# Performance work log

Measured on AMD Instinct MI355X. Metric: run time of the kernel, lower is better.

## Reference

```python
import jax, jax.numpy as jnp
import numpy as np

SELECTED_NUM = 4096
BN_EPS = 1e-5


def _conv1d(x, w, pad):
    # x: [B, C_in, L], w: [C_out, C_in, K]
    return jax.lax.conv_general_dilated(
        x, w, window_strides=(1,), padding=[(pad, pad)],
        dimension_numbers=('NCH', 'OIH', 'NCH'))


def _bn(x, g, b, m, v):
    # eval-mode BatchNorm1d over channel dim of [B, C, L]
    inv = g / jnp.sqrt(v + BN_EPS)
    return x * inv[None, :, None] + (b - m * inv)[None, :, None]


def setup_inputs() -> dict:
    key = jax.random.key(0)
    ks = jax.random.split(key, 16)
    B, N, CODE, NCLS = 4, 262144, 7, 3
    inp = {
        'box_preds': jax.random.normal(ks[0], (B, N, CODE), jnp.float32),
        'cls_preds': jax.random.normal(ks[1], (B, N, NCLS), jnp.float32),
        # conv_share: Conv1d(10,32,3) + BN(32) + ReLU + Conv1d(32,64,3) + BN(64) + ReLU
        'conv1_w': jax.random.normal(ks[2], (32, 10, 3), jnp.float32) * 0.1,
        'bn1_g': jax.random.uniform(ks[3], (32,), jnp.float32, 0.5, 1.5),
        'bn1_b': jax.random.normal(ks[4], (32,), jnp.float32) * 0.1,
        'bn1_m': jax.random.normal(ks[5], (32,), jnp.float32) * 0.1,
        'bn1_v': jax.random.uniform(ks[6], (32,), jnp.float32, 0.5, 1.5),
        'conv2_w': jax.random.normal(ks[7], (64, 32, 3), jnp.float32) * 0.1,
        'bn2_g': jax.random.uniform(ks[8], (64,), jnp.float32, 0.5, 1.5),
        'bn2_b': jax.random.normal(ks[9], (64,), jnp.float32) * 0.1,
        'bn2_m': jax.random.normal(ks[10], (64,), jnp.float32) * 0.1,
        'bn2_v': jax.random.uniform(ks[11], (64,), jnp.float32, 0.5, 1.5),
        # heads: Conv1d(64,5,1,bias=True), Conv1d(64,1,1,bias=True)
        'bin_w': jax.random.normal(ks[12], (5, 64, 1), jnp.float32) * 0.1,
        'bin_b': jnp.full((5,), -float(np.log((1 - 0.01) / 0.01)), jnp.float32),
        'res_w': jax.random.normal(ks[13], (1, 64, 1), jnp.float32) * 0.001,
        'res_b': jnp.zeros((1,), jnp.float32),
    }
    return inp


def reference(box_preds, cls_preds, conv1_w, bn1_g, bn1_b, bn1_m, bn1_v,
              conv2_w, bn2_g, bn2_b, bn2_m, bn2_v, bin_w, bin_b, res_w, res_b):
    # ---- proposal_layer: per-batch sigmoid(max-cls-score) topk + gather ----
    score = jax.nn.sigmoid(jnp.max(cls_preds, axis=-1))          # [B, N]
    _, sel = jax.lax.top_k(score, SELECTED_NUM)                  # [B, K]
    box_sel = jnp.take_along_axis(box_preds, sel[:, :, None], axis=1)  # [B, K, 7]
    cls_sel = jnp.take_along_axis(cls_preds, sel[:, :, None], axis=1)  # [B, K, 3]

    # ---- conv_share + heads over channel-first layout [B, 10, K] ----
    x = jnp.concatenate([box_sel, cls_sel], axis=-1).transpose(0, 2, 1)  # [B, 10, K]
    x = jax.nn.relu(_bn(_conv1d(x, conv1_w, 1), bn1_g, bn1_b, bn1_m, bn1_v))
    x = jax.nn.relu(_bn(_conv1d(x, conv2_w, 1), bn2_g, bn2_b, bn2_m, bn2_v))  # [B, 64, K]

    iou_bin = _conv1d(x, bin_w, 0) + bin_b[None, :, None]        # [B, 5, K]
    iou_res = _conv1d(x, res_w, 0) + res_b[None, :, None]        # [B, 1, K]

    iou_preds_bin = iou_bin.transpose(0, 2, 1)                   # [B, K, 5]
    iou_preds_residual = iou_res.transpose(0, 2, 1)              # [B, K, 1]
    return iou_preds_bin, iou_preds_residual, box_sel, cls_sel
```

## Files before the change

kernel.cpp:

```cpp
#include <hip/hip_runtime.h>
#include <stdint.h>

#define NPTS 262144
#define NB 4
#define KSEL 4096
#define CAP 8192
#define SLICE_LEN 1024
#define CBLK 128
#define HBLK 64
#define NBIN 8192

#define OFF_BITS  0ULL
#define OFF_H13   (4ULL*NPTS*NB)
#define OFF_CTRL  (OFF_H13 + 4ULL*NBIN*NB)
#define OFF_GRANK (OFF_CTRL + 1024ULL)
#define OFF_CAND  (OFF_GRANK + 4ULL*CAP*NB)
#define WS_NEEDED (OFF_CAND + 8ULL*CAP*NB)

#define OBIN 0
#define ORES (NB*KSEL*5)
#define OBOX (ORES + NB*KSEL)
#define OCLS (OBOX + NB*KSEL*7)


__device__ __forceinline__ uint32_t key_of(float mx) {
    uint32_t b = __float_as_uint(mx);
    uint32_t mask = ((int32_t)b >> 31) | 0x80000000u;
    return b ^ mask;
}

__device__ __forceinline__ void suffix_scan_256(volatile uint32_t* part, int tid) {
    #pragma unroll
    for (int off = 1; off < 256; off <<= 1) {
        uint32_t v = part[tid] + ((tid + off < 256) ? part[tid + off] : 0u);
        __syncthreads();
        part[tid] = v;
        __syncthreads();
    }
}

__global__ __launch_bounds__(256) void k_init(uint4* __restrict__ h13v)
{
    h13v[blockIdx.x * 256 + threadIdx.x] = make_uint4(0u, 0u, 0u, 0u);
}

__global__ __launch_bounds__(256) void k_score(
    const float* __restrict__ cls, uint32_t* __restrict__ bits, uint32_t* __restrict__ h13,
    uint32_t* __restrict__ grank, uint32_t* __restrict__ ctrl)
{
    __shared__ uint32_t lh[NBIN];
    for (int i = threadIdx.x; i < NBIN; i += 256) lh[i] = 0;
    __syncthreads();
    int b = blockIdx.y, bx = blockIdx.x;
    for (int it = 0; it < 4; ++it) {
        int chunk = bx * 1024 + it * 256 + threadIdx.x;
        const float4* p = (const float4*)(cls + ((size_t)b * NPTS + (size_t)chunk * 4) * 3);
        float4 v0 = p[0], v1 = p[1], v2 = p[2];
        uint4 o;
        o.x = key_of(fmaxf(fmaxf(v0.x, v0.y), v0.z));
        o.y = key_of(fmaxf(fmaxf(v0.w, v1.x), v1.y));
        o.z = key_of(fmaxf(fmaxf(v1.z, v1.w), v2.x));
        o.w = key_of(fmaxf(fmaxf(v2.y, v2.z), v2.w));
        ((uint4*)(bits + (size_t)b * NPTS))[chunk] = o;
        atomicAdd(&lh[o.x >> 19], 1u);
        atomicAdd(&lh[o.y >> 19], 1u);
        atomicAdd(&lh[o.z >> 19], 1u);
        atomicAdd(&lh[o.w >> 19], 1u);
    }
    if (bx == 1) {
        uint4* zg = (uint4*)(grank + (size_t)b * CAP);
        #pragma unroll
        for (int i = 0; i < 8; ++i) zg[threadIdx.x + i * 256] = make_uint4(0u, 0u, 0u, 0u);
    } else if (bx == 2 && threadIdx.x == 0) {
        ctrl[b * 16 + 3] = 0u;
    }
    __syncthreads();
    uint32_t* h13b = h13 + (size_t)b * NBIN;
    for (int i = threadIdx.x; i < NBIN; i += 256) {
        uint32_t c = lh[i];
        if (c) atomicAdd(&h13b[i], c);
    }
}

__global__ __launch_bounds__(256) void k_compact(
    const uint32_t* __restrict__ bits, const uint32_t* __restrict__ h13,
    uint32_t* __restrict__ ctrl, uint64_t* __restrict__ cand)
{
    __shared__ uint32_t bins[NBIN];
    __shared__ uint32_t part[257];
    __shared__ uint32_t segS, Ts;
    __shared__ uint32_t wbase[4];
    int b = blockIdx.y, bx = blockIdx.x;
    int tid = threadIdx.x;
    const uint4* src = (const uint4*)(h13 + (size_t)b * NBIN);
    for (int i = tid; i < NBIN / 4; i += 256) ((uint4*)bins)[i] = src[i];
    __syncthreads();
    {
        uint32_t s = 0;
        int base2 = tid * 32;
        #pragma unroll
        for (int j = 0; j < 32; ++j) s += bins[base2 + j];
        part[tid] = s;
        if (tid == 0) part[256] = 0u;
    }
    __syncthreads();
    suffix_scan_256(part, tid);
    {
        uint32_t si = part[tid], sn = part[tid + 1];
        if (si >= (uint32_t)KSEL && sn < (uint32_t)KSEL) segS = (uint32_t)tid;
    }
    __syncthreads();
    if (tid < 32) {
        uint32_t seg = segS;
        uint32_t above = part[seg + 1];
        uint32_t cnt = above;
        for (int j = 31; j >= tid; --j) cnt += bins[seg * 32 + j];
        uint32_t cntn = cnt - bins[seg * 32 + tid];
        if (cnt >= (uint32_t)KSEL && cntn < (uint32_t)KSEL)
            Ts = seg * 32 + (uint32_t)tid;
    }
    __syncthreads();
    const uint32_t T = Ts;
    const int lane = tid & 63, wave = tid >> 6;
    const uint64_t lmask = (1ull << lane) - 1ull;

    int chunk0 = bx * 512 + tid;
    const uint4* sb = (const uint4*)(bits + (size_t)b * NPTS);
    uint4 v0 = sb[chunk0];
    uint4 v1 = sb[chunk0 + 256];
    uint32_t ks[8] = {v0.x, v0.y, v0.z, v0.w, v1.x, v1.y, v1.z, v1.w};
    bool sel[8];
    #pragma unroll
    for (int i = 0; i < 8; ++i) sel[i] = (ks[i] >> 19) >= T;

    uint32_t wsum = 0;
    #pragma unroll
    for (int i = 0; i < 8; ++i) wsum += (uint32_t)__popcll(__ballot(sel[i]));
    if (lane == 0) wbase[wave] = wsum;
    __syncthreads();
    if (tid == 0) {
        uint32_t c0 = wbase[0], c1 = wbase[1], c2 = wbase[2], c3 = wbase[3];
        uint32_t tot = c0 + c1 + c2 + c3;
        uint32_t base = tot ? atomicAdd(&ctrl[b * 16 + 3], tot) : 0u;
        wbase[0] = base;
        wbase[1] = base + c0;
        wbase[2] = base + c0 + c1;
        wbase[3] = base + c0 + c1 + c2;
    }
    __syncthreads();
    uint32_t off = wbase[wave];
    #pragma unroll
    for (int i = 0; i < 8; ++i) {
        uint64_t m = __ballot(sel[i]);
        if (sel[i]) {
            uint32_t pos = off + (uint32_t)__popcll(m & lmask);
            uint32_t n = (uint32_t)(chunk0 + (i < 4 ? 0 : 256)) * 4 + (uint32_t)(i & 3);
            if (pos < CAP)
                cand[(size_t)b * CAP + pos] = ((uint64_t)(~ks[i]) << 32) | (uint64_t)n;
        }
        off += (uint32_t)__popcll(m);
    }
}

__global__ __launch_bounds__(256) void k_rank1(
    const uint64_t* __restrict__ cand, const uint32_t* __restrict__ ctrl,
    uint32_t* __restrict__ grank)
{
    __shared__ uint64_t keys[SLICE_LEN];
    int b = blockIdx.z;
    uint32_t C = ctrl[b * 16 + 3];
    if (C > CAP) C = CAP;
    uint32_t ig0 = blockIdx.x * 256;
    uint32_t sk0 = blockIdx.y * SLICE_LEN;
    if (ig0 >= C || sk0 >= C) return;
    uint32_t nk = C - sk0; if (nk > SLICE_LEN) nk = SLICE_LEN;
    const uint64_t* cb = cand + (size_t)b * CAP;
    for (uint32_t i = threadIdx.x; i < nk; i += 256) keys[i] = cb[sk0 + i];
    __syncthreads();
    uint32_t item = ig0 + threadIdx.x;
    if (item >= C) return;
    uint64_t me = cb[item];
    uint32_t r = 0;
    #pragma unroll 16
    for (uint32_t i = 0; i < nk; ++i) r += (keys[i] < me) ? 1u : 0u;
    atomicAdd(&grank[b * CAP + item], r);
}

__global__ __launch_bounds__(256) void k_rank2(
    const uint64_t* __restrict__ cand, const uint32_t* __restrict__ ctrl,
    const uint32_t* __restrict__ grank,
    const float* __restrict__ box, const float* __restrict__ cls, float* __restrict__ out)
{
    int b = blockIdx.y;
    uint32_t C = ctrl[b * 16 + 3];
    if (C > CAP) C = CAP;
    uint32_t item = blockIdx.x * 256 + threadIdx.x;
    if (blockIdx.x * 256 >= C) return;
    if (item >= C) return;
    uint64_t me = cand[(size_t)b * CAP + item];
    uint32_t rank = grank[b * CAP + item];
    if (rank < KSEL) {
        uint32_t n = (uint32_t)me;
        const float* bp = box + ((size_t)b * NPTS + n) * 7;
        float* ob = out + OBOX + ((size_t)b * KSEL + rank) * 7;
        #pragma unroll
        for (int c = 0; c < 7; ++c) ob[c] = bp[c];
        const float* cp = cls + ((size_t)b * NPTS + n) * 3;
        float* oc = out + OCLS + ((size_t)b * KSEL + rank) * 3;
        #pragma unroll
        for (int c = 0; c < 3; ++c) oc[c] = cp[c];
    }
}

__global__ __launch_bounds__(256) void k_conv(
    const float* __restrict__ c1w, const float* __restrict__ g1v, const float* __restrict__ b1v,
    const float* __restrict__ m1v, const float* __restrict__ v1v,
    const float* __restrict__ c2w, const float* __restrict__ g2v, const float* __restrict__ b2v,
    const float* __restrict__ m2v, const float* __restrict__ v2v,
    const float* __restrict__ binw, const float* __restrict__ binb,
    const float* __restrict__ resw, const float* __restrict__ resb,
    float* __restrict__ out)
{
    __shared__ __align__(16) float w1s[960];
    __shared__ __align__(16) float b1s[32];
    __shared__ __align__(16) float w2s[6144];
    __shared__ __align__(16) float b2s[64];
    __shared__ __align__(16) float hws[6][64];
    __shared__ __align__(16) float xin[10][80];
    __shared__ __align__(16) float x1s[32][68];
    __shared__ __align__(16) float x2t[64][68];

    int tid = threadIdx.x;
    int b = blockIdx.y;
    int tile0 = blockIdx.x * 64;
    const float* boxsel = out + OBOX + (size_t)b * KSEL * 7;
    const float* clssel = out + OCLS + (size_t)b * KSEL * 3;

    for (int t = tid; t < 960; t += 256) {
        int c = t / 30, r = t - c * 30, i = r / 3, tap = r - i * 3;
        float inv = g1v[c] * rsqrtf(v1v[c] + 1e-5f);
        w1s[(i * 3 + tap) * 32 + c] = c1w[t] * inv;
    }
    if (tid < 32) {
        float inv = g1v[tid] * rsqrtf(v1v[tid] + 1e-5f);
        b1s[tid] = b1v[tid] - m1v[tid] * inv;
    }
    for (int t = tid; t < 6144; t += 256) {
        int o = t / 96, r = t - o * 96, i = r / 3, tap = r - i * 3;
        float inv = g2v[o] * rsqrtf(v2v[o] + 1e-5f);
        w2s[(i * 3 + tap) * 64 + o] = c2w[t] * inv;
    }
    if (tid >= 64 && tid < 128) {
        int o = tid - 64;
        float inv = g2v[o] * rsqrtf(v2v[o] + 1e-5f);
        b2s[o] = b2v[o] - m2v[o] * inv;
    }
    for (int t = tid; t < 384; t += 256)
        ((float*)hws)[t] = (t < 320) ? binw[t] : resw[t - 320];

    for (int u = tid; u < 680; u += 256) {
        int c = u / 68, k2 = u - c * 68;
        int g = tile0 + k2 - 2;
        float val = 0.f;
        if (g >= 0 && g < KSEL) val = (c < 7) ? boxsel[g * 7 + c] : clssel[g * 3 + (c - 7)];
        xin[c][k2] = val;
    }
    __syncthreads();

    {
        int c = tid & 31, kg = tid >> 5;
        int k0 = kg * 9;
        int nk = 66 - k0; if (nk > 9) nk = 9;
        float a[9];
        #pragma unroll
        for (int kk = 0; kk < 9; ++kk) a[kk] = b1s[c];
        #pragma unroll 2
        for (int i = 0; i < 10; ++i) {
            float xv[11];
            #pragma unroll
            for (int j = 0; j < 11; ++j) xv[j] = xin[i][k0 + j];
            #pragma unroll
            for (int tap = 0; tap < 3; ++tap) {
                float w = w1s[(i * 3 + tap) * 32 + c];
                #pragma unroll
                for (int kk = 0; kk < 9; ++kk) a[kk] = fmaf(w, xv[kk + tap], a[kk]);
            }
        }
        for (int kk = 0; kk < nk; ++kk) {
            int k = k0 + kk, gp = tile0 + k - 1;
            x1s[c][k] = (gp >= 0 && gp < KSEL) ? fmaxf(a[kk], 0.f) : 0.f;
        }
    }
    __syncthreads();

    {
        int o = tid & 63, pg = tid >> 6;
        int p0 = pg * 16;
        float acc[16];
        float bz = b2s[o];
        #pragma unroll
        for (int kk = 0; kk < 16; ++kk) acc[kk] = bz;
        #pragma unroll 4
        for (int i = 0; i < 32; ++i) {
            float4 xq[5];
            const float4* xr = (const float4*)&x1s[i][p0];
            #pragma unroll
            for (int q = 0; q < 5; ++q) xq[q] = xr[q];
            const float* xf = (const float*)xq;
            float w0 = w2s[(i * 3 + 0) * 64 + o];
            float w1 = w2s[(i * 3 + 1) * 64 + o];
            float w2 = w2s[(i * 3 + 2) * 64 + o];
            #pragma unroll
            for (int kk = 0; kk < 16; ++kk) {
                float t0 = fmaf(w0, xf[kk], acc[kk]);
                t0 = fmaf(w1, xf[kk + 1], t0);
                acc[kk] = fmaf(w2, xf[kk + 2], t0);
            }
        }
        #pragma unroll
        for (int kk = 0; kk < 16; ++kk)
            x2t[p0 + kk][o] = fmaxf(acc[kk], 0.f);
    }
    __syncthreads();

    {
        int p = tid & 63, g = tid >> 6;
        const float4* xr = (const float4*)&x2t[p][0];
        const float4* hw4 = (const float4*)hws;
        size_t gpos = (size_t)b * KSEL + (size_t)(tile0 + p);
        if (g < 2) {
            int j0 = g * 2, j1 = j0 + 1;
            float s0 = 0.f, s1 = 0.f;
            #pragma unroll
            for (int q = 0; q < 16; ++q) {
                float4 xv = xr[q];
                float4 wa = hw4[j0 * 16 + q];
                float4 wb = hw4[j1 * 16 + q];
                s0 = fmaf(xv.x, wa.x, s0); s0 = fmaf(xv.y, wa.y, s0);
                s0 = fmaf(xv.z, wa.z, s0); s0 = fmaf(xv.w, wa.w, s0);
                s1 = fmaf(xv.x, wb.x, s1); s1 = fmaf(xv.y, wb.y, s1);
                s1 = fmaf(xv.z, wb.z, s1); s1 = fmaf(xv.w, wb.w, s1);
            }
            out[OBIN + gpos * 5 + j0] = s0 + binb[j0];
            out[OBIN + gpos * 5 + j1] = s1 + binb[j1];
        } else {
            int j = (g == 2) ? 4 : 5;
            float s = 0.f;
            #pragma unroll
            for (int q = 0; q < 16; ++q) {
                float4 xv = xr[q];
                float4 wa = hw4[j * 16 + q];
                s = fmaf(xv.x, wa.x, s); s = fmaf(xv.y, wa.y, s);
                s = fmaf(xv.z, wa.z, s); s = fmaf(xv.w, wa.w, s);
            }
            if (g == 2) out[OBIN + gpos * 5 + 4] = s + binb[4];
            else        out[ORES + gpos]         = s + resb[0];
        }
    }
}

extern "C" void kernel_launch(void* const* d_in, const int* in_sizes, int n_in,
                              void* d_out, int out_size, void* d_ws, size_t ws_size,
                              hipStream_t stream)
{
    const float* box  = (const float*)d_in[0];
    const float* cls  = (const float*)d_in[1];
    const float* c1w  = (const float*)d_in[2];
    const float* g1   = (const float*)d_in[3];
    const float* b1   = (const float*)d_in[4];
    const float* m1   = (const float*)d_in[5];
    const float* v1   = (const float*)d_in[6];
    const float* c2w  = (const float*)d_in[7];
    const float* g2   = (const float*)d_in[8];
    const float* b2   = (const float*)d_in[9];
    const float* m2   = (const float*)d_in[10];
    const float* v2   = (const float*)d_in[11];
    const float* binw = (const float*)d_in[12];
    const float* binb = (const float*)d_in[13];
    const float* resw = (const float*)d_in[14];
    const float* resb = (const float*)d_in[15];
    float* out = (float*)d_out;
    char* ws = (char*)d_ws;
    if (ws_size < WS_NEEDED) return;

    uint32_t* bits  = (uint32_t*)(ws + OFF_BITS);
    uint32_t* h13   = (uint32_t*)(ws + OFF_H13);
    uint32_t* ctrl  = (uint32_t*)(ws + OFF_CTRL);
    uint32_t* grank = (uint32_t*)(ws + OFF_GRANK);
    uint64_t* cand  = (uint64_t*)(ws + OFF_CAND);

    k_init<<<(NBIN * NB) / 1024, 256, 0, stream>>>((uint4*)h13);
    k_score<<<dim3(HBLK, NB), 256, 0, stream>>>(cls, bits, h13, grank, ctrl);
    k_compact<<<dim3(CBLK, NB), 256, 0, stream>>>(bits, h13, ctrl, cand);
    k_rank1<<<dim3(CAP / 256, 8, NB), 256, 0, stream>>>(cand, ctrl, grank);
    k_rank2<<<dim3(CAP / 256, NB), 256, 0, stream>>>(cand, ctrl, grank, box, cls, out);
    k_conv<<<dim3(64, NB), 256, 0, stream>>>(c1w, g1, b1, m1, v1, c2w, g2, b2, m2, v2,
                                             binw, binb, resw, resb, out);
}
```

Measured before the change: 68.48 us.

## Fuse threshold search and gather via last-block-done atomic counters

Moves the histogram threshold search into the score kernel: the last block per batch, found with an atomic counter, scans the global histogram and writes the threshold to ctrl. This stops every compact block from reloading and rescanning the full histogram. The rank and gather kernels are merged the same way: the last slice block per item group does the gather. One kernel launch is removed, in exchange for extra fences, atomics and a serial tail on the last block.

```diff
diff --git a/kernel.cpp b/kernel.cpp
--- a/kernel.cpp
+++ b/kernel.cpp
@@ -39,9 +39,11 @@
     }
 }
 
-__global__ __launch_bounds__(256) void k_init(uint4* __restrict__ h13v)
-{
-    h13v[blockIdx.x * 256 + threadIdx.x] = make_uint4(0u, 0u, 0u, 0u);
+__global__ __launch_bounds__(256) void k_init(uint4* __restrict__ h13v, uint32_t* __restrict__ ctrl)
+{
+    int bx = blockIdx.x, tid = threadIdx.x;
+    h13v[bx * 256 + tid] = make_uint4(0u, 0u, 0u, 0u);
+    if (bx == 0) ctrl[tid] = 0u;
 }
 
 __global__ __launch_bounds__(256) void k_score(
@@ -49,11 +51,14 @@
     uint32_t* __restrict__ grank, uint32_t* __restrict__ ctrl)
 {
     __shared__ uint32_t lh[NBIN];
-    for (int i = threadIdx.x; i < NBIN; i += 256) lh[i] = 0;
-    __syncthreads();
-    int b = blockIdx.y, bx = blockIdx.x;
+    __shared__ uint32_t part[257];
+    __shared__ uint32_t segS;
+    __shared__ int amLastS;
+    int b = blockIdx.y, bx = blockIdx.x, tid = threadIdx.x;
+    for (int i = tid; i < NBIN; i += 256) lh[i] = 0;
+    __syncthreads();
     for (int it = 0; it < 4; ++it) {
-        int chunk = bx * 1024 + it * 256 + threadIdx.x;
+        int chunk = bx * 1024 + it * 256 + tid;
         const float4* p = (const float4*)(cls + ((size_t)b * NPTS + (size_t)chunk * 4) * 3);
         float4 v0 = p[0], v1 = p[1], v2 = p[2];
         uint4 o;
@@ -70,36 +75,30 @@
     if (bx == 1) {
         uint4* zg = (uint4*)(grank + (size_t)b * CAP);
         #pragma unroll
-        for (int i = 0; i < 8; ++i) zg[threadIdx.x + i * 256] = make_uint4(0u, 0u, 0u, 0u);
-    } else if (bx == 2 && threadIdx.x == 0) {
-        ctrl[b * 16 + 3] = 0u;
+        for (int i = 0; i < 8; ++i) zg[tid + i * 256] = make_uint4(0u, 0u, 0u, 0u);
     }
     __syncthreads();
     uint32_t* h13b = h13 + (size_t)b * NBIN;
-    for (int i = threadIdx.x; i < NBIN; i += 256) {
+    for (int i = tid; i < NBIN; i += 256) {
         uint32_t c = lh[i];
         if (c) atomicAdd(&h13b[i], c);
     }
-}
-
-__global__ __launch_bounds__(256) void k_compact(
-    const uint32_t* __restrict__ bits, const uint32_t* __restrict__ h13,
-    uint32_t* __restrict__ ctrl, uint64_t* __restrict__ cand)
-{
-    __shared__ uint32_t bins[NBIN];
-    __shared__ uint32_t part[257];
-    __shared__ uint32_t segS, Ts;
-    __shared__ uint32_t wbase[4];
-    int b = blockIdx.y, bx = blockIdx.x;
-    int tid = threadIdx.x;
-    const uint4* src = (const uint4*)(h13 + (size_t)b * NBIN);
-    for (int i = tid; i < NBIN / 4; i += 256) ((uint4*)bins)[i] = src[i];
+    __threadfence();
+    if (tid == 0) {
+        uint32_t r = atomicAdd(&ctrl[b * 64 + 15], 1u);
+        amLastS = (r == (uint32_t)(HBLK - 1));
+    }
+    __syncthreads();
+    if (!amLastS) return;
+
+    for (int i = tid; i < NBIN / 4; i += 256)
+        ((uint4*)lh)[i] = ((const uint4*)h13b)[i];
     __syncthreads();
     {
         uint32_t s = 0;
         int base2 = tid * 32;
         #pragma unroll
-        for (int j = 0; j < 32; ++j) s += bins[base2 + j];
+        for (int j = 0; j < 32; ++j) s += lh[base2 + j];
         part[tid] = s;
         if (tid == 0) part[256] = 0u;
     }
@@ -114,13 +113,19 @@
         uint32_t seg = segS;
         uint32_t above = part[seg + 1];
         uint32_t cnt = above;
-        for (int j = 31; j >= tid; --j) cnt += bins[seg * 32 + j];
-        uint32_t cntn = cnt - bins[seg * 32 + tid];
+        for (int j = 31; j >= tid; --j) cnt += lh[seg * 32 + j];
+        uint32_t cntn = cnt - lh[seg * 32 + tid];
         if (cnt >= (uint32_t)KSEL && cntn < (uint32_t)KSEL)
-            Ts = seg * 32 + (uint32_t)tid;
-    }
-    __syncthreads();
-    const uint32_t T = Ts;
+            ctrl[b * 64 + 2] = seg * 32 + (uint32_t)tid;
+    }
+}
+
+__global__ __launch_bounds__(256) void k_compact(
+    const uint32_t* __restrict__ bits, uint32_t* __restrict__ ctrl, uint64_t* __restrict__ cand)
+{
+    __shared__ uint32_t wbase[4];
+    int b = blockIdx.y, bx = blockIdx.x, tid = threadIdx.x;
+    const uint32_t T = ctrl[b * 64 + 2];
     const int lane = tid & 63, wave = tid >> 6;
     const uint64_t lmask = (1ull << lane) - 1ull;
 
@@ -141,7 +146,7 @@
     if (tid == 0) {
         uint32_t c0 = wbase[0], c1 = wbase[1], c2 = wbase[2], c3 = wbase[3];
         uint32_t tot = c0 + c1 + c2 + c3;
-        uint32_t base = tot ? atomicAdd(&ctrl[b * 16 + 3], tot) : 0u;
+        uint32_t base = tot ? atomicAdd(&ctrl[b * 64 + 3], tot) : 0u;
         wbase[0] = base;
         wbase[1] = base + c0;
         wbase[2] = base + c0 + c1;
@@ -162,53 +167,52 @@
     }
 }
 
-__global__ __launch_bounds__(256) void k_rank1(
-    const uint64_t* __restrict__ cand, const uint32_t* __restrict__ ctrl,
-    uint32_t* __restrict__ grank)
+__global__ __launch_bounds__(256) void k_rank(
+    const uint64_t* __restrict__ cand, uint32_t* __restrict__ ctrl,
+    uint32_t* __restrict__ grank,
+    const float* __restrict__ box, const float* __restrict__ cls, float* __restrict__ out)
 {
     __shared__ uint64_t keys[SLICE_LEN];
-    int b = blockIdx.z;
-    uint32_t C = ctrl[b * 16 + 3];
+    __shared__ int lastS;
+    int b = blockIdx.z, tid = threadIdx.x;
+    uint32_t C = ctrl[b * 64 + 3];
     if (C > CAP) C = CAP;
-    uint32_t ig0 = blockIdx.x * 256;
+    uint32_t ig = blockIdx.x;
+    uint32_t ig0 = ig * 256;
     uint32_t sk0 = blockIdx.y * SLICE_LEN;
     if (ig0 >= C || sk0 >= C) return;
+    uint32_t Sact = (C + SLICE_LEN - 1) / SLICE_LEN;
     uint32_t nk = C - sk0; if (nk > SLICE_LEN) nk = SLICE_LEN;
     const uint64_t* cb = cand + (size_t)b * CAP;
-    for (uint32_t i = threadIdx.x; i < nk; i += 256) keys[i] = cb[sk0 + i];
-    __syncthreads();
-    uint32_t item = ig0 + threadIdx.x;
-    if (item >= C) return;
-    uint64_t me = cb[item];
+    for (uint32_t i = tid; i < nk; i += 256) keys[i] = cb[sk0 + i];
+    __syncthreads();
+    uint32_t item = ig0 + tid;
+    uint64_t me = (item < C) ? cb[item] : ~0ull;
     uint32_t r = 0;
     #pragma unroll 16
     for (uint32_t i = 0; i < nk; ++i) r += (keys[i] < me) ? 1u : 0u;
-    atomicAdd(&grank[b * CAP + item], r);
-}
-
-__global__ __launch_bounds__(256) void k_rank2(
-    const uint64_t* __restrict__ cand, const uint32_t* __restrict__ ctrl,
-    const uint32_t* __restrict__ grank,
-    const float* __restrict__ box, const float* __restrict__ cls, float* __restrict__ out)
-{
-    int b = blockIdx.y;
-    uint32_t C = ctrl[b * 16 + 3];
-    if (C > CAP) C = CAP;
-    uint32_t item = blockIdx.x * 256 + threadIdx.x;
-    if (blockIdx.x * 256 >= C) return;
-    if (item >= C) return;
-    uint64_t me = cand[(size_t)b * CAP + item];
-    uint32_t rank = grank[b * CAP + item];
-    if (rank < KSEL) {
-        uint32_t n = (uint32_t)me;
-        const float* bp = box + ((size_t)b * NPTS + n) * 7;
-        float* ob = out + OBOX + ((size_t)b * KSEL + rank) * 7;
-        #pragma unroll
-        for (int c = 0; c < 7; ++c) ob[c] = bp[c];
-        const float* cp = cls + ((size_t)b * NPTS + n) * 3;
-        float* oc = out + OCLS + ((size_t)b * KSEL + rank) * 3;
-        #pragma unroll
-        for (int c = 0; c < 3; ++c) oc[c] = cp[c];
+    if (item < C) atomicAdd(&grank[b * CAP + item], r);
+    __syncthreads();
+    __threadfence();
+    if (tid == 0) {
+        uint32_t old = atomicAdd(&ctrl[b * 64 + 16 + ig], 1u);
+        lastS = (old == Sact - 1);
+    }
+    __syncthreads();
+    if (!lastS) return;
+    if (item < C) {
+        uint32_t rank = grank[b * CAP + item];
+        if (rank < KSEL) {
+            uint32_t n = (uint32_t)cb[item];
+            const float* bp = box + ((size_t)b * NPTS + n) * 7;
+            float* ob = out + OBOX + ((size_t)b * KSEL + rank) * 7;
+            #pragma unroll
+            for (int c = 0; c < 7; ++c) ob[c] = bp[c];
+            const float* cp = cls + ((size_t)b * NPTS + n) * 3;
+            float* oc = out + OCLS + ((size_t)b * KSEL + rank) * 3;
+            #pragma unroll
+            for (int c = 0; c < 3; ++c) oc[c] = cp[c];
+        }
     }
 }
 
@@ -389,11 +393,10 @@
     uint32_t* grank = (uint32_t*)(ws + OFF_GRANK);
     uint64_t* cand  = (uint64_t*)(ws + OFF_CAND);
 
-    k_init<<<(NBIN * NB) / 1024, 256, 0, stream>>>((uint4*)h13);
+    k_init<<<(NBIN * NB) / 1024, 256, 0, stream>>>((uint4*)h13, ctrl);
     k_score<<<dim3(HBLK, NB), 256, 0, stream>>>(cls, bits, h13, grank, ctrl);
-    k_compact<<<dim3(CBLK, NB), 256, 0, stream>>>(bits, h13, ctrl, cand);
-    k_rank1<<<dim3(CAP / 256, 8, NB), 256, 0, stream>>>(cand, ctrl, grank);
-    k_rank2<<<dim3(CAP / 256, NB), 256, 0, stream>>>(cand, ctrl, grank, box, cls, out);
+    k_compact<<<dim3(CBLK, NB), 256, 0, stream>>>(bits, ctrl, cand);
+    k_rank<<<dim3(CAP / 256, 8, NB), 256, 0, stream>>>(cand, ctrl, grank, box, cls, out);
     k_conv<<<dim3(64, NB), 256, 0, stream>>>(c1w, g1, b1, m1, v1, c2w, g2, b2, m2, v2,
                                              binw, binb, resw, resb, out);
 }
```

After: 99.30 us. 1.45x slower.

## Bucket candidates by histogram bin to restrict rank counting to same-bin keys

Applied to the files above, without the earlier changes.

Candidates are now written into bin-sorted positions in compaction. Each slot comes from a per-bin global counter plus a suffix sum of the histogram, replacing the single atomic cursor. The rank kernel then only compares each candidate against keys in its own bin range, not all candidates, and writes ranks directly without atomics. This drops the quadratic all-pairs comparison and the grank zeroing. The cost is extra shared memory, per-bin global atomics, and a serial suffix loop per selected element in compaction.

```diff
diff --git a/kernel.cpp b/kernel.cpp
--- a/kernel.cpp
+++ b/kernel.cpp
@@ -12,10 +12,12 @@
 
 #define OFF_BITS  0ULL
 #define OFF_H13   (4ULL*NPTS*NB)
-#define OFF_CTRL  (OFF_H13 + 4ULL*NBIN*NB)
-#define OFF_GRANK (OFF_CTRL + 1024ULL)
-#define OFF_CAND  (OFF_GRANK + 4ULL*CAP*NB)
-#define WS_NEEDED (OFF_CAND + 8ULL*CAP*NB)
+#define OFF_SFX   (OFF_H13 + 4ULL*NBIN*NB)
+#define OFF_BCNT  (OFF_SFX + 4ULL*NBIN*NB)
+#define OFF_CTRL  (OFF_BCNT + 4ULL*NBIN*NB)
+#define OFF_CAND  (OFF_CTRL + 1024ULL)
+#define OFF_GRANK (OFF_CAND + 8ULL*CAP*NB)
+#define WS_NEEDED (OFF_GRANK + 4ULL*CAP*NB)
 
 #define OBIN 0
 #define ORES (NB*KSEL*5)
@@ -39,21 +41,23 @@
     }
 }
 
-__global__ __launch_bounds__(256) void k_init(uint4* __restrict__ h13v)
-{
-    h13v[blockIdx.x * 256 + threadIdx.x] = make_uint4(0u, 0u, 0u, 0u);
+__global__ __launch_bounds__(256) void k_init(uint4* __restrict__ h13v, uint4* __restrict__ bcntv)
+{
+    int bx = blockIdx.x, tid = threadIdx.x;
+    uint4 z = make_uint4(0u, 0u, 0u, 0u);
+    if (bx < 32) h13v[bx * 256 + tid] = z;
+    else         bcntv[(bx - 32) * 256 + tid] = z;
 }
 
 __global__ __launch_bounds__(256) void k_score(
-    const float* __restrict__ cls, uint32_t* __restrict__ bits, uint32_t* __restrict__ h13,
-    uint32_t* __restrict__ grank, uint32_t* __restrict__ ctrl)
+    const float* __restrict__ cls, uint32_t* __restrict__ bits, uint32_t* __restrict__ h13)
 {
     __shared__ uint32_t lh[NBIN];
-    for (int i = threadIdx.x; i < NBIN; i += 256) lh[i] = 0;
-    __syncthreads();
-    int b = blockIdx.y, bx = blockIdx.x;
+    int b = blockIdx.y, bx = blockIdx.x, tid = threadIdx.x;
+    for (int i = tid; i < NBIN; i += 256) lh[i] = 0;
+    __syncthreads();
     for (int it = 0; it < 4; ++it) {
-        int chunk = bx * 1024 + it * 256 + threadIdx.x;
+        int chunk = bx * 1024 + it * 256 + tid;
         const float4* p = (const float4*)(cls + ((size_t)b * NPTS + (size_t)chunk * 4) * 3);
         float4 v0 = p[0], v1 = p[1], v2 = p[2];
         uint4 o;
@@ -67,16 +71,9 @@
         atomicAdd(&lh[o.z >> 19], 1u);
         atomicAdd(&lh[o.w >> 19], 1u);
     }
-    if (bx == 1) {
-        uint4* zg = (uint4*)(grank + (size_t)b * CAP);
-        #pragma unroll
-        for (int i = 0; i < 8; ++i) zg[threadIdx.x + i * 256] = make_uint4(0u, 0u, 0u, 0u);
-    } else if (bx == 2 && threadIdx.x == 0) {
-        ctrl[b * 16 + 3] = 0u;
-    }
     __syncthreads();
     uint32_t* h13b = h13 + (size_t)b * NBIN;
-    for (int i = threadIdx.x; i < NBIN; i += 256) {
+    for (int i = tid; i < NBIN; i += 256) {
         uint32_t c = lh[i];
         if (c) atomicAdd(&h13b[i], c);
     }
@@ -84,16 +81,17 @@
 
 __global__ __launch_bounds__(256) void k_compact(
     const uint32_t* __restrict__ bits, const uint32_t* __restrict__ h13,
+    uint32_t* __restrict__ sfx, uint32_t* __restrict__ bcnt,
     uint32_t* __restrict__ ctrl, uint64_t* __restrict__ cand)
 {
     __shared__ uint32_t bins[NBIN];
+    __shared__ uint32_t lha[NBIN];
     __shared__ uint32_t part[257];
     __shared__ uint32_t segS, Ts;
-    __shared__ uint32_t wbase[4];
-    int b = blockIdx.y, bx = blockIdx.x;
-    int tid = threadIdx.x;
+    int b = blockIdx.y, bx = blockIdx.x, tid = threadIdx.x;
     const uint4* src = (const uint4*)(h13 + (size_t)b * NBIN);
     for (int i = tid; i < NBIN / 4; i += 256) ((uint4*)bins)[i] = src[i];
+    for (int i = tid; i < NBIN; i += 256) lha[i] = 0;
     __syncthreads();
     {
         uint32_t s = 0;
@@ -121,8 +119,19 @@
     }
     __syncthreads();
     const uint32_t T = Ts;
-    const int lane = tid & 63, wave = tid >> 6;
-    const uint64_t lmask = (1ull << lane) - 1ull;
+    if (bx == 0) {
+        uint32_t run = part[tid + 1];
+        uint32_t* sb2 = sfx + (size_t)b * NBIN + tid * 32;
+        for (int j = 31; j >= 0; --j) {
+            run += bins[tid * 32 + j];
+            sb2[j] = run;
+        }
+        if (tid == 0) {
+            uint32_t seg = T >> 5, run2 = part[seg + 1];
+            for (int j = 31; j >= (int)(T & 31u); --j) run2 += bins[seg * 32 + j];
+            ctrl[b * 64 + 3] = (run2 > (uint32_t)CAP) ? (uint32_t)CAP : run2;
+        }
+    }
 
     int chunk0 = bx * 512 + tid;
     const uint4* sb = (const uint4*)(bits + (size_t)b * NPTS);
@@ -133,57 +142,78 @@
     #pragma unroll
     for (int i = 0; i < 8; ++i) sel[i] = (ks[i] >> 19) >= T;
 
-    uint32_t wsum = 0;
     #pragma unroll
-    for (int i = 0; i < 8; ++i) wsum += (uint32_t)__popcll(__ballot(sel[i]));
-    if (lane == 0) wbase[wave] = wsum;
-    __syncthreads();
-    if (tid == 0) {
-        uint32_t c0 = wbase[0], c1 = wbase[1], c2 = wbase[2], c3 = wbase[3];
-        uint32_t tot = c0 + c1 + c2 + c3;
-        uint32_t base = tot ? atomicAdd(&ctrl[b * 16 + 3], tot) : 0u;
-        wbase[0] = base;
-        wbase[1] = base + c0;
-        wbase[2] = base + c0 + c1;
-        wbase[3] = base + c0 + c1 + c2;
-    }
-    __syncthreads();
-    uint32_t off = wbase[wave];
+    for (int i = 0; i < 8; ++i)
+        if (sel[i]) atomicAdd(&lha[ks[i] >> 19], 1u);
+    __syncthreads();
+    {
+        uint32_t* bc = bcnt + (size_t)b * NBIN;
+        for (int i = tid; i < NBIN; i += 256) {
+            uint32_t c = lha[i];
+            if (c) lha[i] = atomicAdd(&bc[i], c);
+        }
+    }
+    __syncthreads();
     #pragma unroll
     for (int i = 0; i < 8; ++i) {
-        uint64_t m = __ballot(sel[i]);
         if (sel[i]) {
-            uint32_t pos = off + (uint32_t)__popcll(m & lmask);
+            uint32_t bin = ks[i] >> 19;
+            uint32_t lo = 0;
+            if (bin < NBIN - 1) {
+                uint32_t x = bin + 1, seg = x >> 5;
+                lo = part[seg + 1];
+                for (int j = 31; j >= (int)(x & 31u); --j) lo += bins[seg * 32 + j];
+            }
+            uint32_t pos = lo + atomicAdd(&lha[bin], 1u);
             uint32_t n = (uint32_t)(chunk0 + (i < 4 ? 0 : 256)) * 4 + (uint32_t)(i & 3);
             if (pos < CAP)
                 cand[(size_t)b * CAP + pos] = ((uint64_t)(~ks[i]) << 32) | (uint64_t)n;
         }
-        off += (uint32_t)__popcll(m);
     }
 }
 
 __global__ __launch_bounds__(256) void k_rank1(
     const uint64_t* __restrict__ cand, const uint32_t* __restrict__ ctrl,
-    uint32_t* __restrict__ grank)
+    const uint32_t* __restrict__ sfx, uint32_t* __restrict__ grank)
 {
     __shared__ uint64_t keys[SLICE_LEN];
-    int b = blockIdx.z;
-    uint32_t C = ctrl[b * 16 + 3];
+    __shared__ uint32_t loMinS, hiMaxS;
+    int b = blockIdx.y, tid = threadIdx.x;
+    uint32_t C = ctrl[b * 64 + 3];
     if (C > CAP) C = CAP;
     uint32_t ig0 = blockIdx.x * 256;
-    uint32_t sk0 = blockIdx.y * SLICE_LEN;
-    if (ig0 >= C || sk0 >= C) return;
-    uint32_t nk = C - sk0; if (nk > SLICE_LEN) nk = SLICE_LEN;
+    if (ig0 >= C) return;
     const uint64_t* cb = cand + (size_t)b * CAP;
-    for (uint32_t i = threadIdx.x; i < nk; i += 256) keys[i] = cb[sk0 + i];
-    __syncthreads();
-    uint32_t item = ig0 + threadIdx.x;
-    if (item >= C) return;
-    uint64_t me = cb[item];
-    uint32_t r = 0;
-    #pragma unroll 16
-    for (uint32_t i = 0; i < nk; ++i) r += (keys[i] < me) ? 1u : 0u;
-    atomicAdd(&grank[b * CAP + item], r);
+    uint32_t item = ig0 + tid;
+    bool valid = (item < C);
+    uint64_t me = valid ? cb[item] : ~0ull;
+    uint32_t ksv = ~(uint32_t)(me >> 32);
+    uint32_t bin = ksv >> 19;
+    const uint32_t* sfb = sfx + (size_t)b * NBIN;
+    uint32_t lo = 0, hi = 0;
+    if (valid) {
+        lo = (bin >= NBIN - 1) ? 0u : sfb[bin + 1];
+        hi = sfb[bin];
+        if (lo > C) lo = C;
+        if (hi > C) hi = C;
+    }
+    if (tid == 0) { loMinS = 0xFFFFFFFFu; hiMaxS = 0u; }
+    __syncthreads();
+    if (valid) { atomicMin(&loMinS, lo); atomicMax(&hiMaxS, hi); }
+    __syncthreads();
+    uint32_t r = lo;
+    for (uint32_t s0 = loMinS; s0 < hiMaxS; s0 += SLICE_LEN) {
+        uint32_t nk = hiMaxS - s0; if (nk > SLICE_LEN) nk = SLICE_LEN;
+        for (uint32_t i = tid; i < nk; i += 256) keys[i] = cb[s0 + i];
+        __syncthreads();
+        if (valid && hi > s0 && lo < s0 + nk) {
+            uint32_t a = (lo > s0) ? (lo - s0) : 0u;
+            uint32_t e = hi - s0; if (e > nk) e = nk;
+            for (uint32_t i = a; i < e; ++i) r += (keys[i] < me) ? 1u : 0u;
+        }
+        __syncthreads();
+    }
+    if (valid) grank[b * CAP + item] = r;
 }
 
 __global__ __launch_bounds__(256) void k_rank2(
@@ -192,7 +222,7 @@
     const float* __restrict__ box, const float* __restrict__ cls, float* __restrict__ out)
 {
     int b = blockIdx.y;
-    uint32_t C = ctrl[b * 16 + 3];
+    uint32_t C = ctrl[b * 64 + 3];
     if (C > CAP) C = CAP;
     uint32_t item = blockIdx.x * 256 + threadIdx.x;
     if (blockIdx.x * 256 >= C) return;
@@ -385,14 +415,16 @@
 
     uint32_t* bits  = (uint32_t*)(ws + OFF_BITS);
     uint32_t* h13   = (uint32_t*)(ws + OFF_H13);
+    uint32_t* sfx   = (uint32_t*)(ws + OFF_SFX);
+    uint32_t* bcnt  = (uint32_t*)(ws + OFF_BCNT);
     uint32_t* ctrl  = (uint32_t*)(ws + OFF_CTRL);
+    uint64_t* cand  = (uint64_t*)(ws + OFF_CAND);
     uint32_t* grank = (uint32_t*)(ws + OFF_GRANK);
-    uint64_t* cand  = (uint64_t*)(ws + OFF_CAND);
-
-    k_init<<<(NBIN * NB) / 1024, 256, 0, stream>>>((uint4*)h13);
-    k_score<<<dim3(HBLK, NB), 256, 0, stream>>>(cls, bits, h13, grank, ctrl);
-    k_compact<<<dim3(CBLK, NB), 256, 0, stream>>>(bits, h13, ctrl, cand);
-    k_rank1<<<dim3(CAP / 256, 8, NB), 256, 0, stream>>>(cand, ctrl, grank);
+
+    k_init<<<64, 256, 0, stream>>>((uint4*)h13, (uint4*)bcnt);
+    k_score<<<dim3(HBLK, NB), 256, 0, stream>>>(cls, bits, h13);
+    k_compact<<<dim3(CBLK, NB), 256, 0, stream>>>(bits, h13, sfx, bcnt, ctrl, cand);
+    k_rank1<<<dim3(CAP / 256, NB), 256, 0, stream>>>(cand, ctrl, sfx, grank);
     k_rank2<<<dim3(CAP / 256, NB), 256, 0, stream>>>(cand, ctrl, grank, box, cls, out);
     k_conv<<<dim3(64, NB), 256, 0, stream>>>(c1w, g1, b1, m1, v1, c2w, g2, b2, m2, v2,
                                              binw, binb, resw, resb, out);
```

Measured after the change: 179.1 us. 162% more time.
